# Performance work log

Measured on AMD Instinct MI355X. Metric: run time of the kernel, lower is better.

Reference implementation:

```python
import jax, jax.numpy as jnp
from jax import lax
import numpy as np

B, T, F, H, L = 256, 512, 64, 128, 2


def lstm_layer(x, W_ih, W_hh, b_ih, b_hh):
    """PyTorch-style LSTM layer. x:[B,T,I]; W_ih:[4H,I]; W_hh:[4H,H]. Gate order i,f,g,o."""
    b = x.shape[0]
    h_dim = W_hh.shape[1]
    # Precompute input contribution for all timesteps: [B,T,4H]
    xg = jnp.einsum('bti,gi->btg', x, W_ih) + b_ih + b_hh

    def step(carry, xg_t):
        h, c = carry
        g = xg_t + h @ W_hh.T  # [B,4H]
        i, f, gg, o = jnp.split(g, 4, axis=-1)
        c = jax.nn.sigmoid(f) * c + jax.nn.sigmoid(i) * jnp.tanh(gg)
        h = jax.nn.sigmoid(o) * jnp.tanh(c)
        return (h, c), h

    h0 = jnp.zeros((b, h_dim), x.dtype)
    c0 = jnp.zeros((b, h_dim), x.dtype)
    (hT, _), hs = lax.scan(step, (h0, c0), jnp.swapaxes(xg, 0, 1))  # hs:[T,B,H]
    return jnp.swapaxes(hs, 0, 1), hT


def setup_inputs() -> dict:
    key = jax.random.key(0)
    ks = iter(jax.random.split(key, 32))
    s = 0.05
    d = {"x": jax.random.normal(next(ks), (B, T, F), jnp.float32)}
    # encoder: layer0 input F, layer1 input H; decoder: both layers input H
    for name, in0 in (("enc", F), ("dec", H)):
        for l in range(L):
            I = in0 if l == 0 else H
            d[f"{name}{l}_Wih"] = jax.random.normal(next(ks), (4 * H, I), jnp.float32) * s
            d[f"{name}{l}_Whh"] = jax.random.normal(next(ks), (4 * H, H), jnp.float32) * s
            d[f"{name}{l}_bih"] = jax.random.normal(next(ks), (4 * H,), jnp.float32) * s
            d[f"{name}{l}_bhh"] = jax.random.normal(next(ks), (4 * H,), jnp.float32) * s
    d["W_out"] = jax.random.normal(next(ks), (F, H), jnp.float32) * s
    d["b_out"] = jnp.zeros((F,), jnp.float32)
    return d


def reference(x,
              enc0_Wih, enc0_Whh, enc0_bih, enc0_bhh,
              enc1_Wih, enc1_Whh, enc1_bih, enc1_bhh,
              dec0_Wih, dec0_Whh, dec0_bih, dec0_bhh,
              dec1_Wih, dec1_Whh, dec1_bih, dec1_bhh,
              W_out, b_out):
    enc = [(enc0_Wih, enc0_Whh, enc0_bih, enc0_bhh),
           (enc1_Wih, enc1_Whh, enc1_bih, enc1_bhh)]
    dec = [(dec0_Wih, dec0_Whh, dec0_bih, dec0_bhh),
           (dec1_Wih, dec1_Whh, dec1_bih, dec1_bhh)]
    # Encoder: stacked LSTM, keep last layer's final hidden state
    h = x
    hT = None
    for p in enc:
        h, hT = lstm_layer(h, *p)
    # Repeat final hidden over sequence
    dec_in = jnp.broadcast_to(hT[:, None, :], (x.shape[0], x.shape[1], hT.shape[-1]))
    # Decoder: stacked LSTM over full output sequence
    d = dec_in
    for p in dec:
        d, _ = lstm_layer(d, *p)
    # Linear projection back to feature space
    return jnp.einsum('bth,fh->btf', d, W_out) + b_out
```

## Files before the change

### kernel.cpp

```cpp
#include <hip/hip_runtime.h>
#include <cstddef>

namespace {

typedef _Float16 half_t;
typedef _Float16 half2_t __attribute__((ext_vector_type(2)));
typedef _Float16 f16x4 __attribute__((ext_vector_type(4)));
typedef _Float16 f16x8 __attribute__((ext_vector_type(8)));
typedef float f32x4 __attribute__((ext_vector_type(4)));

constexpr int NB = 256;
constexpr int NT = 512;
constexpr int NH = 128;
constexpr int NG = 512;

__device__ __forceinline__ float sigm(float x) { return 1.0f / (1.0f + __expf(-x)); }
__device__ __forceinline__ float tanh_(float x) { return 2.0f / (1.0f + __expf(-2.0f * x)) - 1.0f; }
__device__ __forceinline__ float dot4(float4 w, float4 v, float acc) {
  return fmaf(w.x, v.x, fmaf(w.y, v.y, fmaf(w.z, v.z, fmaf(w.w, v.w, acc))));
}
__device__ __forceinline__ float fdot2(half2_t a, half2_t b, float c) {
  return __builtin_amdgcn_fdot2(a, b, c, false);
}
__device__ __forceinline__ half2_t lo2(f16x8 v, int q) {
  half2_t r; r[0] = v[2 * q]; r[1] = v[2 * q + 1]; return r;
}
__device__ __forceinline__ void pinv8(f16x8& x) { asm volatile("" : "+v"(x)); }

__global__ void cvt_kernel(const float* __restrict__ s, half_t* __restrict__ d, int n4) {
  int i = blockIdx.x * blockDim.x + threadIdx.x;
  if (i < n4) {
    float4 v = reinterpret_cast<const float4*>(s)[i];
    f16x4 hv = {(half_t)v.x, (half_t)v.y, (half_t)v.z, (half_t)v.w};
    reinterpret_cast<f16x4*>(d)[i] = hv;
  }
}

template <int K, bool AF32, bool F32OUT>
__global__ __launch_bounds__(256) void xg_gemm(
    const void* __restrict__ Ap, const float* __restrict__ Bw,
    const float* __restrict__ b0, const float* __restrict__ b1,
    half_t* __restrict__ Ch, float* __restrict__ Cf, int Nstr)
{
  __shared__ __align__(16) half_t Atile[128 * K];
  __shared__ __align__(16) half_t Btile[64 * K];
  const int tid = threadIdx.x;
  const int m0 = blockIdx.x * 128;
  const int n0 = blockIdx.y * 64;
  char* Ab = (char*)Atile;
  char* Bb = (char*)Btile;

  if (AF32) {
    const float* Af = (const float*)Ap;
    for (int idx = tid; idx < 128 * K / 4; idx += 256) {
      int row = idx / (K / 4), o = idx % (K / 4);
      float4 v = *(const float4*)(Af + (size_t)(m0 + row) * K + 4 * o);
      f16x4 hv = {(half_t)v.x, (half_t)v.y, (half_t)v.z, (half_t)v.w};
      int byte = ((row * K + 4 * o) * 2) ^ ((row & 7) << 4);
      *(f16x4*)(Ab + byte) = hv;
    }
  } else {
    const half_t* Ah = (const half_t*)Ap;
    for (int idx = tid; idx < 128 * K / 8; idx += 256) {
      int row = idx / (K / 8), o = idx % (K / 8);
      uint4 v = *(const uint4*)(Ah + (size_t)(m0 + row) * K + 8 * o);
      int byte = ((row * K + 8 * o) * 2) ^ ((row & 7) << 4);
      *(uint4*)(Ab + byte) = v;
    }
  }
  for (int idx = tid; idx < 64 * K / 4; idx += 256) {
    int row = idx / (K / 4), o = idx % (K / 4);
    float4 v = *(const float4*)(Bw + (size_t)(n0 + row) * K + 4 * o);
    f16x4 hv = {(half_t)v.x, (half_t)v.y, (half_t)v.z, (half_t)v.w};
    int byte = ((row * K + 4 * o) * 2) ^ ((row & 7) << 4);
    *(f16x4*)(Bb + byte) = hv;
  }
  __syncthreads();

  const int lane = tid & 63, w = tid >> 6;
  const int r16 = lane & 15, koff = (lane >> 4) * 8;
  f32x4 acc[2][4];
#pragma unroll
  for (int fm = 0; fm < 2; ++fm)
#pragma unroll
    for (int fn = 0; fn < 4; ++fn) acc[fm][fn] = (f32x4){0.f, 0.f, 0.f, 0.f};

#pragma unroll
  for (int ks = 0; ks < K / 32; ++ks) {
    f16x8 a[2], bf[4];
#pragma unroll
    for (int fm = 0; fm < 2; ++fm) {
      int row = w * 32 + fm * 16 + r16;
      int byte = ((row * K + ks * 32 + koff) * 2) ^ ((row & 7) << 4);
      a[fm] = *(const f16x8*)(Ab + byte);
    }
#pragma unroll
    for (int fn = 0; fn < 4; ++fn) {
      int row = fn * 16 + r16;
      int byte = ((row * K + ks * 32 + koff) * 2) ^ ((row & 7) << 4);
      bf[fn] = *(const f16x8*)(Bb + byte);
    }
#pragma unroll
    for (int fm = 0; fm < 2; ++fm)
#pragma unroll
      for (int fn = 0; fn < 4; ++fn)
        acc[fm][fn] = __builtin_amdgcn_mfma_f32_16x16x32_f16(a[fm], bf[fn], acc[fm][fn], 0, 0, 0);
  }

#pragma unroll
  for (int fm = 0; fm < 2; ++fm)
#pragma unroll
    for (int fn = 0; fn < 4; ++fn) {
      int n = n0 + fn * 16 + r16;
      float bb = (b0 ? b0[n] : 0.f) + (b1 ? b1[n] : 0.f);
#pragma unroll
      for (int q = 0; q < 4; ++q) {
        int m = m0 + w * 32 + fm * 16 + (lane >> 4) * 4 + q;
        float val = acc[fm][fn][q] + bb;
        if (F32OUT) Cf[(size_t)m * Nstr + n] = val;
        else        Ch[(size_t)m * Nstr + n] = (half_t)val;
      }
    }
}

template <int MODE>
__global__ __attribute__((amdgpu_flat_work_group_size(512, 512)))
__attribute__((amdgpu_waves_per_eu(2, 2))) void rec_kernel(
    const half_t* __restrict__ xg,
    const float* __restrict__ hT_in,
    const float* __restrict__ WihD,
    const float* __restrict__ bih, const float* __restrict__ bhh,
    const half_t* __restrict__ Whh,
    half_t* __restrict__ seq_out,
    float* __restrict__ hT_out)
{
  const int b = blockIdx.x;
  const int tid = threadIdx.x;
  const int j = tid >> 2;
  const int kq = tid & 3;

  __shared__ __align__(16) half_t hbuf[2][4][48];
  __shared__ __align__(16) half_t xgs[2][8][NG];
  __shared__ float xgc[NG];
  __shared__ float hinf[NH];

  f16x8 wh8[4][4];
#pragma unroll
  for (int gi = 0; gi < 4; ++gi) {
    const f16x8* p = reinterpret_cast<const f16x8*>(Whh + (size_t)(gi * NH + j) * NH + kq * 32);
#pragma unroll
    for (int r = 0; r < 4; ++r) wh8[gi][r] = p[r];
  }
#pragma unroll
  for (int gi = 0; gi < 4; ++gi)
#pragma unroll
    for (int r = 0; r < 4; ++r) pinv8(wh8[gi][r]);

  if (tid < NH) hbuf[0][tid >> 5][tid & 31] = (half_t)0.0f;
  float c = 0.0f;

  if (MODE == 2) {
    if (tid < NH) hinf[tid] = hT_in[(size_t)b * NH + tid];
    __syncthreads();
    float a0 = bih[tid] + bhh[tid], a1 = 0.f, a2 = 0.f, a3 = 0.f;
    const float4* wr = (const float4*)(WihD + (size_t)tid * NH);
    const float4* hv = (const float4*)hinf;
#pragma unroll
    for (int k = 0; k < 8; ++k) {
      a0 = dot4(wr[4 * k + 0], hv[4 * k + 0], a0);
      a1 = dot4(wr[4 * k + 1], hv[4 * k + 1], a1);
      a2 = dot4(wr[4 * k + 2], hv[4 * k + 2], a2);
      a3 = dot4(wr[4 * k + 3], hv[4 * k + 3], a3);
    }
    xgc[tid] = (a0 + a1) + (a2 + a3);
    __syncthreads();
  }

  half_t g[8];
  const half_t* xrow = nullptr;
  if (MODE != 2) {
    xrow = xg + (size_t)b * NT * NG + tid;
#pragma unroll
    for (int s = 0; s < 8; ++s) g[s] = xrow[(size_t)s * NG];
  }

  for (int ch = 0; ch < NT / 8; ++ch) {
    if (MODE != 2) {
#pragma unroll
      for (int s = 0; s < 8; ++s) xgs[ch & 1][s][tid] = g[s];
      if (ch < NT / 8 - 1) {
#pragma unroll
        for (int s = 0; s < 8; ++s) g[s] = xrow[(size_t)((ch + 1) * 8 + s) * NG];
      }
      __syncthreads();
    }

#pragma unroll 1
    for (int tt = 0; tt < 8; ++tt) {
      const int t = ch * 8 + tt;
      const int p = t & 1;

      float a0 = 0.f, a1 = 0.f, a2 = 0.f, a3 = 0.f;
      const f16x8* hv8 = reinterpret_cast<const f16x8*>(&hbuf[p][kq][0]);
#pragma unroll
      for (int r8 = 0; r8 < 4; ++r8) {
        const f16x8 H = hv8[r8];
        const half2_t h0 = lo2(H, 0), h1 = lo2(H, 1), h2 = lo2(H, 2), h3 = lo2(H, 3);
        {
          const f16x8 W = wh8[0][r8];
          const half2_t w0 = lo2(W, 0), w1 = lo2(W, 1), w2 = lo2(W, 2), w3 = lo2(W, 3);
          a0 = fdot2(w0, h0, a0); a0 = fdot2(w1, h1, a0);
          a0 = fdot2(w2, h2, a0); a0 = fdot2(w3, h3, a0);
        }
        {
          const f16x8 W = wh8[1][r8];
          const half2_t w0 = lo2(W, 0), w1 = lo2(W, 1), w2 = lo2(W, 2), w3 = lo2(W, 3);
          a1 = fdot2(w0, h0, a1); a1 = fdot2(w1, h1, a1);
          a1 = fdot2(w2, h2, a1); a1 = fdot2(w3, h3, a1);
        }
        {
          const f16x8 W = wh8[2][r8];
          const half2_t w0 = lo2(W, 0), w1 = lo2(W, 1), w2 = lo2(W, 2), w3 = lo2(W, 3);
          a2 = fdot2(w0, h0, a2); a2 = fdot2(w1, h1, a2);
          a2 = fdot2(w2, h2, a2); a2 = fdot2(w3, h3, a2);
        }
        {
          const f16x8 W = wh8[3][r8];
          const half2_t w0 = lo2(W, 0), w1 = lo2(W, 1), w2 = lo2(W, 2), w3 = lo2(W, 3);
          a3 = fdot2(w0, h0, a3); a3 = fdot2(w1, h1, a3);
          a3 = fdot2(w2, h2, a3); a3 = fdot2(w3, h3, a3);
        }
      }
      a0 += __shfl_xor(a0, 1, 4); a0 += __shfl_xor(a0, 2, 4);
      a1 += __shfl_xor(a1, 1, 4); a1 += __shfl_xor(a1, 2, 4);
      a2 += __shfl_xor(a2, 1, 4); a2 += __shfl_xor(a2, 2, 4);
      a3 += __shfl_xor(a3, 1, 4); a3 += __shfl_xor(a3, 2, 4);

      float xi, xf, xgg, xo;
      if (MODE == 2) {
        xi = xgc[j]; xf = xgc[j + 128]; xgg = xgc[j + 256]; xo = xgc[j + 384];
      } else {
        const half_t* xb = &xgs[ch & 1][tt][0];
        xi = (float)xb[j]; xf = (float)xb[j + 128];
        xgg = (float)xb[j + 256]; xo = (float)xb[j + 384];
      }

      const float ig = sigm(a0 + xi);
      const float fg = sigm(a1 + xf);
      const float gg = tanh_(a2 + xgg);
      const float og = sigm(a3 + xo);
      c = fmaf(fg, c, ig * gg);
      const float h = og * tanh_(c);

      if (kq == 0) {
        hbuf[p ^ 1][j >> 5][j & 31] = (half_t)h;
        if (MODE != 1) seq_out[((size_t)b * NT + t) * NH + j] = (half_t)h;
        else if (t == NT - 1) hT_out[(size_t)b * NH + j] = h;
      }
      __syncthreads();
    }
  }
}

}

extern "C" void kernel_launch(void* const* d_in, const int* in_sizes, int n_in,
                              void* d_out, int out_size, void* d_ws, size_t ws_size,
                              hipStream_t stream) {
  (void)in_sizes; (void)n_in; (void)out_size; (void)ws_size;

  const float* x     = (const float*)d_in[0];
  const float* e0Wih = (const float*)d_in[1];
  const float* e0Whh = (const float*)d_in[2];
  const float* e0bih = (const float*)d_in[3];
  const float* e0bhh = (const float*)d_in[4];
  const float* e1Wih = (const float*)d_in[5];
  const float* e1Whh = (const float*)d_in[6];
  const float* e1bih = (const float*)d_in[7];
  const float* e1bhh = (const float*)d_in[8];
  const float* d0Wih = (const float*)d_in[9];
  const float* d0Whh = (const float*)d_in[10];
  const float* d0bih = (const float*)d_in[11];
  const float* d0bhh = (const float*)d_in[12];
  const float* d1Wih = (const float*)d_in[13];
  const float* d1Whh = (const float*)d_in[14];
  const float* d1bih = (const float*)d_in[15];
  const float* d1bhh = (const float*)d_in[16];
  const float* Wout  = (const float*)d_in[17];
  const float* bout  = (const float*)d_in[18];
  float* out = (float*)d_out;

  half_t* whh0 = (half_t*)d_ws;
  half_t* whh1 = whh0 + 512 * 128;
  half_t* whh2 = whh1 + 512 * 128;
  half_t* whh3 = whh2 + 512 * 128;
  half_t* seqA = whh3 + 512 * 128;
  half_t* xgb  = seqA + (size_t)NB * NT * NH;
  float*  hT   = (float*)(xgb + (size_t)NB * NT * NG);

  cvt_kernel<<<64, 256, 0, stream>>>(e0Whh, whh0, 512 * 128 / 4);
  cvt_kernel<<<64, 256, 0, stream>>>(e1Whh, whh1, 512 * 128 / 4);
  cvt_kernel<<<64, 256, 0, stream>>>(d0Whh, whh2, 512 * 128 / 4);
  cvt_kernel<<<64, 256, 0, stream>>>(d1Whh, whh3, 512 * 128 / 4);

  const int M = NB * NT;
  dim3 gX(M / 128, NG / 64), gP(M / 128, 1), blkG(256);
  dim3 gR(NB), blkR(512);

  xg_gemm<64, true, false><<<gX, blkG, 0, stream>>>(x, e0Wih, e0bih, e0bhh, xgb, nullptr, NG);
  rec_kernel<0><<<gR, blkR, 0, stream>>>(xgb, nullptr, nullptr, nullptr, nullptr, whh0, seqA, nullptr);

  xg_gemm<128, false, false><<<gX, blkG, 0, stream>>>(seqA, e1Wih, e1bih, e1bhh, xgb, nullptr, NG);
  rec_kernel<1><<<gR, blkR, 0, stream>>>(xgb, nullptr, nullptr, nullptr, nullptr, whh1, nullptr, hT);

  rec_kernel<2><<<gR, blkR, 0, stream>>>(nullptr, hT, d0Wih, d0bih, d0bhh, whh2, seqA, nullptr);

  xg_gemm<128, false, false><<<gX, blkG, 0, stream>>>(seqA, d1Wih, d1bih, d1bhh, xgb, nullptr, NG);
  rec_kernel<0><<<gR, blkR, 0, stream>>>(xgb, nullptr, nullptr, nullptr, nullptr, whh3, seqA, nullptr);

  xg_gemm<128, false, true><<<gP, blkG, 0, stream>>>(seqA, Wout, bout, nullptr, nullptr, out, 64);
}
```

Baseline: 2.012 ms.

## Pack two batch rows per recurrent block with 1024 threads

The recurrent LSTM kernel now processes two batch sequences per workgroup of 1024 threads, halving the grid size, with shared buffers duplicated per half. The intent is to amortize per-block overhead and share resident weights' cache traffic. It trades fewer active CUs, a larger block-wide barrier each timestep, and a tighter register budget from the waves-per-EU change.

```diff
diff --git a/kernel.cpp b/kernel.cpp
--- a/kernel.cpp
+++ b/kernel.cpp
@@ -124,8 +124,8 @@
 }
 
 template <int MODE>
-__global__ __attribute__((amdgpu_flat_work_group_size(512, 512)))
-__attribute__((amdgpu_waves_per_eu(2, 2))) void rec_kernel(
+__global__ __attribute__((amdgpu_flat_work_group_size(1024, 1024)))
+__attribute__((amdgpu_waves_per_eu(4, 4))) void rec_kernel(
     const half_t* __restrict__ xg,
     const float* __restrict__ hT_in,
     const float* __restrict__ WihD,
@@ -134,15 +134,17 @@
     half_t* __restrict__ seq_out,
     float* __restrict__ hT_out)
 {
-  const int b = blockIdx.x;
   const int tid = threadIdx.x;
-  const int j = tid >> 2;
-  const int kq = tid & 3;
-
-  __shared__ __align__(16) half_t hbuf[2][4][48];
-  __shared__ __align__(16) half_t xgs[2][8][NG];
-  __shared__ float xgc[NG];
-  __shared__ float hinf[NH];
+  const int hf = tid >> 9;
+  const int t5 = tid & 511;
+  const int b = blockIdx.x * 2 + hf;
+  const int j = t5 >> 2;
+  const int kq = t5 & 3;
+
+  __shared__ __align__(16) half_t hbuf[2][2][4][48];
+  __shared__ __align__(16) half_t xgs[2][2][8][NG];
+  __shared__ float xgc[2][NG];
+  __shared__ float hinf[2][NH];
 
   f16x8 wh8[4][4];
 #pragma unroll
@@ -156,15 +158,15 @@
 #pragma unroll
     for (int r = 0; r < 4; ++r) pinv8(wh8[gi][r]);
 
-  if (tid < NH) hbuf[0][tid >> 5][tid & 31] = (half_t)0.0f;
+  if (t5 < NH) hbuf[hf][0][t5 >> 5][t5 & 31] = (half_t)0.0f;
   float c = 0.0f;
 
   if (MODE == 2) {
-    if (tid < NH) hinf[tid] = hT_in[(size_t)b * NH + tid];
+    if (t5 < NH) hinf[hf][t5] = hT_in[(size_t)b * NH + t5];
     __syncthreads();
-    float a0 = bih[tid] + bhh[tid], a1 = 0.f, a2 = 0.f, a3 = 0.f;
-    const float4* wr = (const float4*)(WihD + (size_t)tid * NH);
-    const float4* hv = (const float4*)hinf;
+    float a0 = bih[t5] + bhh[t5], a1 = 0.f, a2 = 0.f, a3 = 0.f;
+    const float4* wr = (const float4*)(WihD + (size_t)t5 * NH);
+    const float4* hv = (const float4*)&hinf[hf][0];
 #pragma unroll
     for (int k = 0; k < 8; ++k) {
       a0 = dot4(wr[4 * k + 0], hv[4 * k + 0], a0);
@@ -172,14 +174,14 @@
       a2 = dot4(wr[4 * k + 2], hv[4 * k + 2], a2);
       a3 = dot4(wr[4 * k + 3], hv[4 * k + 3], a3);
     }
-    xgc[tid] = (a0 + a1) + (a2 + a3);
+    xgc[hf][t5] = (a0 + a1) + (a2 + a3);
     __syncthreads();
   }
 
   half_t g[8];
   const half_t* xrow = nullptr;
   if (MODE != 2) {
-    xrow = xg + (size_t)b * NT * NG + tid;
+    xrow = xg + (size_t)b * NT * NG + t5;
 #pragma unroll
     for (int s = 0; s < 8; ++s) g[s] = xrow[(size_t)s * NG];
   }
@@ -187,7 +189,7 @@
   for (int ch = 0; ch < NT / 8; ++ch) {
     if (MODE != 2) {
 #pragma unroll
-      for (int s = 0; s < 8; ++s) xgs[ch & 1][s][tid] = g[s];
+      for (int s = 0; s < 8; ++s) xgs[hf][ch & 1][s][t5] = g[s];
       if (ch < NT / 8 - 1) {
 #pragma unroll
         for (int s = 0; s < 8; ++s) g[s] = xrow[(size_t)((ch + 1) * 8 + s) * NG];
@@ -201,7 +203,7 @@
       const int p = t & 1;
 
       float a0 = 0.f, a1 = 0.f, a2 = 0.f, a3 = 0.f;
-      const f16x8* hv8 = reinterpret_cast<const f16x8*>(&hbuf[p][kq][0]);
+      const f16x8* hv8 = reinterpret_cast<const f16x8*>(&hbuf[hf][p][kq][0]);
 #pragma unroll
       for (int r8 = 0; r8 < 4; ++r8) {
         const f16x8 H = hv8[r8];
@@ -238,9 +240,10 @@
 
       float xi, xf, xgg, xo;
       if (MODE == 2) {
-        xi = xgc[j]; xf = xgc[j + 128]; xgg = xgc[j + 256]; xo = xgc[j + 384];
+        xi = xgc[hf][j]; xf = xgc[hf][j + 128];
+        xgg = xgc[hf][j + 256]; xo = xgc[hf][j + 384];
       } else {
-        const half_t* xb = &xgs[ch & 1][tt][0];
+        const half_t* xb = &xgs[hf][ch & 1][tt][0];
         xi = (float)xb[j]; xf = (float)xb[j + 128];
         xgg = (float)xb[j + 256]; xo = (float)xb[j + 384];
       }
@@ -253,7 +256,7 @@
       const float h = og * tanh_(c);
 
       if (kq == 0) {
-        hbuf[p ^ 1][j >> 5][j & 31] = (half_t)h;
+        hbuf[hf][p ^ 1][j >> 5][j & 31] = (half_t)h;
         if (MODE != 1) seq_out[((size_t)b * NT + t) * NH + j] = (half_t)h;
         else if (t == NT - 1) hT_out[(size_t)b * NH + j] = h;
       }
@@ -305,7 +308,7 @@
 
   const int M = NB * NT;
   dim3 gX(M / 128, NG / 64), gP(M / 128, 1), blkG(256);
-  dim3 gR(NB), blkR(512);
+  dim3 gR(NB / 2), blkR(1024);
 
   xg_gemm<64, true, false><<<gX, blkG, 0, stream>>>(x, e0Wih, e0bih, e0bhh, xgb, nullptr, NG);
   rec_kernel<0><<<gR, blkR, 0, stream>>>(xgb, nullptr, nullptr, nullptr, nullptr, whh0, seqA, nullptr);
```

Result: slower. 3.234 ms (+60.7%).
